# Optimization experiments

Hardware: AMD Instinct MI355X
Metric: run time of the kernel (lower is better)

The kernel has to match this reference:

```python
import jax, jax.numpy as jnp
import numpy as np

B, N, C = 4, 4096, 128

def setup_inputs() -> dict:
    key = jax.random.key(0)
    ks = jax.random.split(key, 7)
    s = 1.0 / np.sqrt(C)
    return {
        "x": jax.random.normal(ks[0], (B, N, C), dtype=jnp.float32),
        "Wq": jax.random.uniform(ks[1], (C, C), jnp.float32, -s, s),
        "bq": jax.random.uniform(ks[2], (C,), jnp.float32, -s, s),
        "Wk": jax.random.uniform(ks[3], (C, C), jnp.float32, -s, s),
        "bk": jax.random.uniform(ks[4], (C,), jnp.float32, -s, s),
        "Wv": jax.random.uniform(ks[5], (C, C), jnp.float32, -s, s),
        "bv": jax.random.uniform(ks[6], (C,), jnp.float32, -s, s),
    }

def reference(x, Wq, bq, Wk, bk, Wv, bv):
    # GELU-activated Q/K/V projections (torch default GELU = exact erf form)
    q = jax.nn.gelu(jnp.einsum("bnc,dc->bnd", x, Wq) + bq, approximate=False)
    k = jax.nn.gelu(jnp.einsum("bnc,dc->bnd", x, Wk) + bk, approximate=False)
    v = jax.nn.gelu(jnp.einsum("bnc,dc->bnd", x, Wv) + bv, approximate=False)
    # Unscaled attention: softmax(Q K^T) V
    scores = jnp.einsum("bnd,bmd->bnm", q, k)  # [B, N, N]
    attn = jax.nn.softmax(scores, axis=-1)
    return jnp.einsum("bnm,bmd->bnd", attn, v)
```

## Files before the change

### kernel.cpp

```cpp
#include <hip/hip_runtime.h>
#include <hip/hip_bf16.h>
#include <math.h>

#define BATCH 4
#define SEQ   4096
#define CDIM  128
#define NROWS (BATCH * SEQ)
#define KVB   32
#define NTILE (SEQ / KVB)
#define KTILE_B 8192
#define VTILE_B 8192
#define STAGE_B (KTILE_B + VTILE_B)
#define LOG2E 1.4426950408889634f

typedef __attribute__((ext_vector_type(4))) float    f32x4;
typedef __attribute__((ext_vector_type(8))) _Float16 half8;
typedef __attribute__((ext_vector_type(4))) short    bf16x4;
typedef __attribute__((ext_vector_type(8))) short    bf16x8;

__device__ __forceinline__ float bf2f(short s) {
  unsigned u = ((unsigned)(unsigned short)s) << 16;
  return __builtin_bit_cast(float, u);
}
__device__ __forceinline__ short f2bf(float f) {
  __hip_bfloat16 h = __float2bfloat16(f);
  return __builtin_bit_cast(short, h);
}
__device__ __forceinline__ float gelu_exact(float v) {
  return 0.5f * v * (1.0f + erff(v * 0.70710678118654752440f));
}
__device__ __forceinline__ float exp2_hw(float x) {
  float r;
  asm("v_exp_f32 %0, %1\n\ts_nop 0" : "=v"(r) : "v"(x));
  return r;
}
__device__ __forceinline__ int kswz_h(int r, int c) {
  int slot  = c >> 3;
  int slotp = (slot & 8) | ((slot ^ r) & 7);
  return r * 128 + slotp * 8 + (c & 7);
}
__device__ __forceinline__ void gl_lds16(const void* g, void* l) {
  __builtin_amdgcn_global_load_lds(
      (const __attribute__((address_space(1))) void*)g,
      (__attribute__((address_space(3))) void*)l, 16, 0, 0);
}

__global__ void wprep_kernel(const float* __restrict__ Wq,
                             const float* __restrict__ Wk,
                             const float* __restrict__ Wv,
                             _Float16* __restrict__ wfrag) {
  int mat = blockIdx.y;
  const float* W = (mat == 0) ? Wq : ((mat == 1) ? Wk : Wv);
  int i = blockIdx.x * 256 + threadIdx.x;
  int d = i >> 7, c = i & 127;
  int nt = d >> 4, qr = d & 15, cc = c >> 5, g = (c >> 3) & 3, j = c & 7;
  wfrag[(size_t)((((mat * 8 + nt) * 4 + cc) * 64) + 16 * g + qr) * 8 + j] =
      (_Float16)W[i];
}

__global__ __launch_bounds__(256) void proj_kernel(
    const float* __restrict__ x, const _Float16* __restrict__ wfrag,
    const float* __restrict__ bq, const float* __restrict__ bk,
    const float* __restrict__ bv,
    _Float16* __restrict__ qfrag, _Float16* __restrict__ kimg,
    short* __restrict__ vimg) {
  __shared__ __align__(16) char pls[16384];
  const int tid = threadIdx.x, wave = tid >> 6, lane = tid & 63;
  const int g = lane >> 4, qr = lane & 15;
  const int row0 = blockIdx.x * 64 + wave * 16;

  half8 xf[4];
#pragma unroll
  for (int c4 = 0; c4 < 4; ++c4) {
    const float* px = x + (size_t)(row0 + qr) * CDIM + 8 * g + 32 * c4;
    f32x4 a = *(const f32x4*)px;
    f32x4 bb = *(const f32x4*)(px + 4);
    half8 hx;
#pragma unroll
    for (int j = 0; j < 4; ++j) { hx[j] = (_Float16)a[j]; hx[4 + j] = (_Float16)bb[j]; }
    xf[c4] = hx;
  }

#pragma unroll
  for (int mat = 0; mat < 3; ++mat) {
    const float* bias = (mat == 0) ? bq : ((mat == 1) ? bk : bv);
    f32x4 acc[8];
#pragma unroll
    for (int nt = 0; nt < 8; ++nt) acc[nt] = (f32x4){0.f, 0.f, 0.f, 0.f};
#pragma unroll
    for (int nt = 0; nt < 8; ++nt)
#pragma unroll
      for (int c4 = 0; c4 < 4; ++c4) {
        half8 wf = *(const half8*)(wfrag +
            ((size_t)(((mat * 8 + nt) * 4 + c4) * 64) + lane) * 8);
        acc[nt] = __builtin_amdgcn_mfma_f32_16x16x32_f16(xf[c4], wf, acc[nt], 0, 0, 0);
      }

    short* ls = (short*)pls;
#pragma unroll
    for (int nt = 0; nt < 8; ++nt) {
      int col = 16 * nt + qr;
      float bi = bias[col];
#pragma unroll
      for (int r = 0; r < 4; ++r) {
        int rl = wave * 16 + 4 * g + r;
        float val = gelu_exact(acc[nt][r] + bi);
        int off;
        short sv;
        if (mat == 0) {
          int lane2 = ((col >> 3) & 3) * 16 + (rl & 15);
          off = ((wave * 4 + (col >> 5)) * 64 + lane2) * 8 + (col & 7);
          sv = __builtin_bit_cast(short, (_Float16)(val * LOG2E));
        } else if (mat == 1) {
          int tl = rl >> 5, rr = rl & 31;
          off = tl * 4096 + kswz_h(rr, col);
          sv = __builtin_bit_cast(short, (_Float16)val);
        } else {
          int tl = rl >> 5, rr = rl & 31;
          off = tl * 4096 + ((rr >> 2) * 128 + col) * 4 + (rr & 3);
          sv = f2bf(val);
        }
        ls[off] = sv;
      }
    }
    __syncthreads();
    char* gdst = (mat == 0) ? (char*)qfrag + (size_t)blockIdx.x * 16384
               : (mat == 1) ? (char*)kimg + (size_t)blockIdx.x * 16384
                            : (char*)vimg + (size_t)blockIdx.x * 16384;
#pragma unroll
    for (int p = 0; p < 4; ++p)
      ((f32x4*)gdst)[tid + 256 * p] = ((const f32x4*)pls)[tid + 256 * p];
    __syncthreads();
  }
}

template <int NSPLIT>
__global__ __launch_bounds__(256, 2) void attn_kernel(
    const _Float16* __restrict__ qfrag, const char* __restrict__ kimg,
    const char* __restrict__ vimg, short* __restrict__ pacc,
    float* __restrict__ pml) {
  __shared__ __align__(16) char smem[2][STAGE_B];
  constexpr int NT = NTILE / NSPLIT;
  const int tid = threadIdx.x, wave = tid >> 6, lane = tid & 63;
  const int g = lane >> 4, qr = lane & 15;

  const int i = blockIdx.x;
  const int stream = i & (4 * NSPLIT - 1);
  const int b = stream / NSPLIT, sp = stream % NSPLIT;
  const int qg = i / (4 * NSPLIT);

  const int t0 = b * 256 + qg * 8 + wave * 2;
  half8 qf[2][4];
#pragma unroll
  for (int qs = 0; qs < 2; ++qs)
#pragma unroll
    for (int c4 = 0; c4 < 4; ++c4)
      qf[qs][c4] = *(const half8*)(qfrag +
          ((size_t)((t0 + qs) * 4 + c4) * 64 + lane) * 8);

  int koff[4];
#pragma unroll
  for (int c4 = 0; c4 < 4; ++c4) {
    int slot = 4 * c4 + g;
    int slotp = (slot & 8) | ((slot ^ qr) & 7);
    koff[c4] = qr * 256 + slotp * 16;
  }
  const int voff = g * 1024 + qr * 8;

  const char* kp = kimg + ((size_t)b * NTILE + sp * NT) * KTILE_B + tid * 16;
  const char* vp = vimg + ((size_t)b * NTILE + sp * NT) * VTILE_B + tid * 16;

  auto stage = [&](char* buf) {
    gl_lds16(kp,        buf + tid * 16);
    gl_lds16(kp + 4096, buf + 4096 + tid * 16);
    gl_lds16(vp,        buf + 8192 + tid * 16);
    gl_lds16(vp + 4096, buf + 12288 + tid * 16);
    kp += KTILE_B;
    vp += VTILE_B;
  };

  f32x4 acc[2][8];
#pragma unroll
  for (int qs = 0; qs < 2; ++qs)
#pragma unroll
    for (int dt = 0; dt < 8; ++dt) acc[qs][dt] = (f32x4){0.f, 0.f, 0.f, 0.f};
  float m[2] = {-INFINITY, -INFINITY}, lsum[2] = {0.f, 0.f};

  stage(smem[0]);

  auto phase = [&](const char* cur, char* other, bool do_stage) {
    asm volatile("s_waitcnt vmcnt(0) lgkmcnt(0)" ::: "memory");
    __builtin_amdgcn_s_barrier();
    if (do_stage) stage(other);

    f32x4 sA[2][2];
#pragma unroll
    for (int s = 0; s < 2; ++s) {
      half8 kf[4];
#pragma unroll
      for (int c4 = 0; c4 < 4; ++c4)
        kf[c4] = *(const half8*)(cur + koff[c4] + s * 4096);
      __builtin_amdgcn_s_setprio(1);
#pragma unroll
      for (int qs = 0; qs < 2; ++qs) {
        f32x4 tac = (f32x4){0.f, 0.f, 0.f, 0.f};
#pragma unroll
        for (int c4 = 0; c4 < 4; ++c4)
          tac = __builtin_amdgcn_mfma_f32_16x16x32_f16(kf[c4], qf[qs][c4], tac, 0, 0, 0);
        sA[qs][s] = tac;
      }
      __builtin_amdgcn_s_setprio(0);
    }

    bf16x4 pf[2][2];
#pragma unroll
    for (int qs = 0; qs < 2; ++qs) {
      float tm = fmaxf(
          fmaxf(fmaxf(sA[qs][0][0], sA[qs][0][1]), fmaxf(sA[qs][0][2], sA[qs][0][3])),
          fmaxf(fmaxf(sA[qs][1][0], sA[qs][1][1]), fmaxf(sA[qs][1][2], sA[qs][1][3])));
      tm = fmaxf(tm, __shfl_xor(tm, 16, 64));
      tm = fmaxf(tm, __shfl_xor(tm, 32, 64));
      if (!__all(tm <= m[qs] + 8.0f)) {
        float mn = fmaxf(m[qs], tm);
        float alpha = exp2_hw(m[qs] - mn);
        m[qs] = mn;
        lsum[qs] *= alpha;
        float af[4];
#pragma unroll
        for (int r = 0; r < 4; ++r) af[r] = __shfl(alpha, 4 * g + r, 64);
#pragma unroll
        for (int dt = 0; dt < 8; ++dt)
#pragma unroll
          for (int r = 0; r < 4; ++r) acc[qs][dt][r] *= af[r];
      }
      float p[8], ps = 0.f;
#pragma unroll
      for (int e = 0; e < 8; ++e) {
        p[e] = exp2_hw(sA[qs][e >> 2][e & 3] - m[qs]);
        ps += p[e];
      }
      ps += __shfl_xor(ps, 16, 64);
      ps += __shfl_xor(ps, 32, 64);
      lsum[qs] += ps;
#pragma unroll
      for (int r = 0; r < 4; ++r) { pf[qs][0][r] = f2bf(p[r]); pf[qs][1][r] = f2bf(p[4 + r]); }
    }

    const char* vb = cur + KTILE_B + voff;
#pragma unroll
    for (int dt = 0; dt < 8; ++dt) {
      bf16x4 v0 = *(const bf16x4*)(vb + dt * 128);
      bf16x4 v1 = *(const bf16x4*)(vb + 4096 + dt * 128);
      __builtin_amdgcn_s_setprio(1);
#pragma unroll
      for (int qs = 0; qs < 2; ++qs) {
        acc[qs][dt] = __builtin_amdgcn_mfma_f32_16x16x16bf16_1k(pf[qs][0], v0, acc[qs][dt], 0, 0, 0);
        acc[qs][dt] = __builtin_amdgcn_mfma_f32_16x16x16bf16_1k(pf[qs][1], v1, acc[qs][dt], 0, 0, 0);
      }
      __builtin_amdgcn_s_setprio(0);
    }
  };

#pragma unroll 1
  for (int it = 0; it < NT / 2; ++it) {
    phase(smem[0], smem[1], true);
    phase(smem[1], smem[0], it != NT / 2 - 1);
  }

  const int lrow0 = qg * 128 + wave * 32;
#pragma unroll
  for (int qs = 0; qs < 2; ++qs) {
#pragma unroll
    for (int dt = 0; dt < 8; ++dt)
#pragma unroll
      for (int r = 0; r < 4; ++r) {
        int grow = b * SEQ + lrow0 + qs * 16 + 4 * g + r;
        pacc[((size_t)sp * NROWS + grow) * CDIM + 16 * dt + qr] =
            f2bf(acc[qs][dt][r]);
      }
    if (g == 0) {
      int grow = b * SEQ + lrow0 + qs * 16 + qr;
      pml[((size_t)sp * NROWS + grow) * 2 + 0] = m[qs];
      pml[((size_t)sp * NROWS + grow) * 2 + 1] = lsum[qs];
    }
  }
}

template <int NSPLIT>
__global__ __launch_bounds__(256) void combine_kernel(
    const short* __restrict__ pacc, const float* __restrict__ pml,
    float* __restrict__ out) {
  int idx = blockIdx.x * 256 + threadIdx.x;
  int row = idx >> 4, c8 = idx & 15;
  float mm[NSPLIT], ll[NSPLIT];
  float M = -INFINITY;
#pragma unroll
  for (int h = 0; h < NSPLIT; ++h) {
    mm[h] = pml[((size_t)h * NROWS + row) * 2 + 0];
    ll[h] = pml[((size_t)h * NROWS + row) * 2 + 1];
    M = fmaxf(M, mm[h]);
  }
  float o[8];
#pragma unroll
  for (int j = 0; j < 8; ++j) o[j] = 0.f;
  float wl = 0.f;
#pragma unroll
  for (int h = 0; h < NSPLIT; ++h) {
    float w = exp2f(mm[h] - M);
    wl += w * ll[h];
    bf16x8 a = ((const bf16x8*)pacc)[((size_t)h * NROWS + row) * 16 + c8];
#pragma unroll
    for (int j = 0; j < 8; ++j) o[j] += w * bf2f(a[j]);
  }
  float inv = 1.0f / wl;
  f32x4 o0 = {o[0] * inv, o[1] * inv, o[2] * inv, o[3] * inv};
  f32x4 o1 = {o[4] * inv, o[5] * inv, o[6] * inv, o[7] * inv};
  ((f32x4*)out)[(size_t)row * 32 + c8 * 2 + 0] = o0;
  ((f32x4*)out)[(size_t)row * 32 + c8 * 2 + 1] = o1;
}

extern "C" void kernel_launch(void* const* d_in, const int* in_sizes, int n_in,
                              void* d_out, int out_size, void* d_ws, size_t ws_size,
                              hipStream_t stream) {
  const float* x  = (const float*)d_in[0];
  const float* Wq = (const float*)d_in[1];
  const float* bq = (const float*)d_in[2];
  const float* Wk = (const float*)d_in[3];
  const float* bk = (const float*)d_in[4];
  const float* Wv = (const float*)d_in[5];
  const float* bv = (const float*)d_in[6];
  float* out = (float*)d_out;

  char* ws = (char*)d_ws;
  _Float16* qfrag = (_Float16*)(ws);
  char*     kimg  = ws + (4u << 20);
  char*     vimg  = ws + (8u << 20);
  _Float16* wfrag = (_Float16*)(ws + (12u << 20));
  char*     tail  = ws + (12u << 20) + (256u << 10);

  const size_t need8 = (12u << 20) + (256u << 10) +
                       (size_t)8 * NROWS * 8 + (size_t)8 * NROWS * CDIM * 2;

  wprep_kernel<<<dim3(64, 3), 256, 0, stream>>>(Wq, Wk, Wv, wfrag);
  proj_kernel<<<NROWS / 64, 256, 0, stream>>>(x, wfrag, bq, bk, bv,
                                              qfrag, (_Float16*)kimg, (short*)vimg);
  if (ws_size >= need8) {
    float* pml  = (float*)tail;
    short* pacc = (short*)(tail + (size_t)8 * NROWS * 8);
    attn_kernel<8><<<1024, 256, 0, stream>>>(qfrag, kimg, vimg, pacc, pml);
    combine_kernel<8><<<NROWS * 16 / 256, 256, 0, stream>>>(pacc, pml, out);
  } else {
    float* pml  = (float*)tail;
    short* pacc = (short*)(tail + (size_t)4 * NROWS * 8);
    attn_kernel<4><<<512, 256, 0, stream>>>(qfrag, kimg, vimg, pacc, pml);
    combine_kernel<4><<<NROWS * 16 / 256, 256, 0, stream>>>(pacc, pml, out);
  }
}
```

Measured before the change: 154.5 us.

## Use 16x16x32 bf16 MFMA for PV and compute softmax row sums via MFMA

Re-lays out the V tile in LDS with a swizzled K-contiguous layout so each lane loads one 8-element bf16 vector, which lets the PV product use the double-K 16x16x32 bf16 MFMA instead of pairs of 16x16x16 ones. The softmax denominator is now accumulated by an MFMA against a vector of ones rather than by per-lane adds and cross-lane shuffles, and it is rescaled alongside the output accumulator. This halves the PV MFMA instruction count and removes the shuffle reductions. In exchange it adds two MFMAs per tile, and the row sum now comes from the bf16-rounded probabilities, which changes numerics slightly.

```diff
diff --git a/kernel.cpp b/kernel.cpp
--- a/kernel.cpp
+++ b/kernel.cpp
@@ -117,7 +117,9 @@
           sv = __builtin_bit_cast(short, (_Float16)val);
         } else {
           int tl = rl >> 5, rr = rl & 31;
-          off = tl * 4096 + ((rr >> 2) * 128 + col) * 4 + (rr & 3);
+          int klin = 8 * ((rr >> 2) & 3) + (rr & 3) + 4 * (rr >> 4);
+          int slotp = (klin >> 3) ^ ((col >> 1) & 3);
+          off = tl * 4096 + col * 32 + slotp * 8 + (klin & 7);
           sv = f2bf(val);
         }
         ls[off] = sv;
@@ -165,7 +167,11 @@
     int slotp = (slot & 8) | ((slot ^ qr) & 7);
     koff[c4] = qr * 256 + slotp * 16;
   }
-  const int voff = g * 1024 + qr * 8;
+  const int voff = qr * 64 + ((g ^ ((qr >> 1) & 3)) << 4);
+
+  bf16x8 ones8;
+#pragma unroll
+  for (int j = 0; j < 8; ++j) ones8[j] = (short)0x3F80;
 
   const char* kp = kimg + ((size_t)b * NTILE + sp * NT) * KTILE_B + tid * 16;
   const char* vp = vimg + ((size_t)b * NTILE + sp * NT) * VTILE_B + tid * 16;
@@ -184,7 +190,8 @@
   for (int qs = 0; qs < 2; ++qs)
 #pragma unroll
     for (int dt = 0; dt < 8; ++dt) acc[qs][dt] = (f32x4){0.f, 0.f, 0.f, 0.f};
-  float m[2] = {-INFINITY, -INFINITY}, lsum[2] = {0.f, 0.f};
+  f32x4 lacc[2] = {(f32x4){0.f, 0.f, 0.f, 0.f}, (f32x4){0.f, 0.f, 0.f, 0.f}};
+  float m[2] = {-INFINITY, -INFINITY};
 
   stage(smem[0]);
 
@@ -212,7 +219,7 @@
       __builtin_amdgcn_s_setprio(0);
     }
 
-    bf16x4 pf[2][2];
+    bf16x8 pf8[2];
 #pragma unroll
     for (int qs = 0; qs < 2; ++qs) {
       float tm = fmaxf(
@@ -224,7 +231,6 @@
         float mn = fmaxf(m[qs], tm);
         float alpha = exp2_hw(m[qs] - mn);
         m[qs] = mn;
-        lsum[qs] *= alpha;
         float af[4];
 #pragma unroll
         for (int r = 0; r < 4; ++r) af[r] = __shfl(alpha, 4 * g + r, 64);
@@ -232,31 +238,23 @@
         for (int dt = 0; dt < 8; ++dt)
 #pragma unroll
           for (int r = 0; r < 4; ++r) acc[qs][dt][r] *= af[r];
-      }
-      float p[8], ps = 0.f;
-#pragma unroll
-      for (int e = 0; e < 8; ++e) {
-        p[e] = exp2_hw(sA[qs][e >> 2][e & 3] - m[qs]);
-        ps += p[e];
-      }
-      ps += __shfl_xor(ps, 16, 64);
-      ps += __shfl_xor(ps, 32, 64);
-      lsum[qs] += ps;
-#pragma unroll
-      for (int r = 0; r < 4; ++r) { pf[qs][0][r] = f2bf(p[r]); pf[qs][1][r] = f2bf(p[4 + r]); }
-    }
-
-    const char* vb = cur + KTILE_B + voff;
+#pragma unroll
+        for (int r = 0; r < 4; ++r) lacc[qs][r] *= af[r];
+      }
+#pragma unroll
+      for (int e = 0; e < 8; ++e)
+        pf8[qs][e] = f2bf(exp2_hw(sA[qs][e >> 2][e & 3] - m[qs]));
+    }
+
+    lacc[0] = __builtin_amdgcn_mfma_f32_16x16x32_bf16(pf8[0], ones8, lacc[0], 0, 0, 0);
+    lacc[1] = __builtin_amdgcn_mfma_f32_16x16x32_bf16(pf8[1], ones8, lacc[1], 0, 0, 0);
+
 #pragma unroll
     for (int dt = 0; dt < 8; ++dt) {
-      bf16x4 v0 = *(const bf16x4*)(vb + dt * 128);
-      bf16x4 v1 = *(const bf16x4*)(vb + 4096 + dt * 128);
+      bf16x8 v = *(const bf16x8*)(cur + KTILE_B + voff + dt * 1024);
       __builtin_amdgcn_s_setprio(1);
-#pragma unroll
-      for (int qs = 0; qs < 2; ++qs) {
-        acc[qs][dt] = __builtin_amdgcn_mfma_f32_16x16x16bf16_1k(pf[qs][0], v0, acc[qs][dt], 0, 0, 0);
-        acc[qs][dt] = __builtin_amdgcn_mfma_f32_16x16x16bf16_1k(pf[qs][1], v1, acc[qs][dt], 0, 0, 0);
-      }
+      acc[0][dt] = __builtin_amdgcn_mfma_f32_16x16x32_bf16(pf8[0], v, acc[0][dt], 0, 0, 0);
+      acc[1][dt] = __builtin_amdgcn_mfma_f32_16x16x32_bf16(pf8[1], v, acc[1][dt], 0, 0, 0);
       __builtin_amdgcn_s_setprio(0);
     }
   };
@@ -281,7 +279,13 @@
     if (g == 0) {
       int grow = b * SEQ + lrow0 + qs * 16 + qr;
       pml[((size_t)sp * NROWS + grow) * 2 + 0] = m[qs];
-      pml[((size_t)sp * NROWS + grow) * 2 + 1] = lsum[qs];
+    }
+    if (qr == 0) {
+#pragma unroll
+      for (int r = 0; r < 4; ++r) {
+        int grow = b * SEQ + lrow0 + qs * 16 + 4 * g + r;
+        pml[((size_t)sp * NROWS + grow) * 2 + 1] = lacc[qs][r];
+      }
     }
   }
 }
```

New measurement: 147.1 us. 1.05x faster.
